# Kernel tuning notes

Measured on AMD Instinct MI355X. Metric: run time of the kernel, lower is better.

Reference implementation:

```python
import jax, jax.numpy as jnp
import numpy as np

N = 50000      # nodes
E = 800000     # edges
D_IN = 512
D_OUT = 512
EDGE_DIM = 3


def setup_inputs() -> dict:
    key = jax.random.key(0)
    k = jax.random.split(key, 6)
    x = jax.random.normal(k[0], (N, D_IN), dtype=jnp.float32)
    edge_index = jax.random.randint(k[1], (2, E), 0, N, dtype=jnp.int64)
    edge_attr = jax.random.normal(k[2], (E, EDGE_DIM), dtype=jnp.float32)
    # xavier-uniform-ish init for linear weights
    lim1 = (6.0 / (D_IN + D_OUT)) ** 0.5
    lin_w = jax.random.uniform(k[3], (D_OUT, D_IN), minval=-lim1, maxval=lim1, dtype=jnp.float32)
    lin_b = jnp.zeros((D_OUT,), dtype=jnp.float32)
    lim2 = (6.0 / (EDGE_DIM + 1)) ** 0.5
    conf_w = jax.random.uniform(k[4], (1, EDGE_DIM), minval=-lim2, maxval=lim2, dtype=jnp.float32)
    conf_b = jnp.zeros((1,), dtype=jnp.float32)
    return {"x": x, "edge_index": edge_index, "edge_attr": edge_attr,
            "lin_w": lin_w, "lin_b": lin_b, "conf_w": conf_w, "conf_b": conf_b}


def reference(x, edge_index, edge_attr, lin_w, lin_b, conf_w, conf_b):
    row, col = edge_index[0], edge_index[1]
    # edge confidence weight: sigmoid(conf_lin(edge_attr)) -> [E]
    edge_weight = jax.nn.sigmoid(edge_attr @ conf_w.T + conf_b)[:, 0]
    # degree of source nodes (count of row occurrences), inverse sqrt with inf/nan -> 0
    deg = jnp.zeros((x.shape[0],), dtype=x.dtype).at[row].add(1.0)
    deg_safe = jnp.where(deg > 0, deg, 1.0)
    deg_inv_sqrt = jnp.where(deg > 0, jax.lax.rsqrt(deg_safe), 0.0)
    norm = deg_inv_sqrt[row] * deg_inv_sqrt[col] * edge_weight  # [E]
    norm = jnp.where(jnp.isnan(norm), 0.0, norm)
    # gather-scale-scatter: out[col] += x[row] * norm
    out = jnp.zeros_like(x).at[col].add(x[row] * norm[:, None])
    return out @ lin_w.T + lin_b
```

## Files before the change

kernel.cpp:

```cpp
#include <hip/hip_runtime.h>

#define NDIM 512

typedef __bf16 bf16x8 __attribute__((ext_vector_type(8)));
typedef float  f32x4  __attribute__((ext_vector_type(4)));

__device__ inline ushort f2bf(float f) {
    uint b = __float_as_uint(f);
    return (ushort)((b + 0x7fffu + ((b >> 16) & 1u)) >> 16);
}
__device__ inline float bflo(uint u) { return __uint_as_float(u << 16); }
__device__ inline float bfhi(uint u) { return __uint_as_float(u & 0xffff0000u); }
__device__ inline uint packbf(float lo, float hi) {
    return ((uint)f2bf(hi) << 16) | (uint)f2bf(lo);
}

__device__ inline void gload16(const ushort* g, ushort* l) {
    __builtin_amdgcn_global_load_lds(
        (const __attribute__((address_space(1))) uint*)g,
        (__attribute__((address_space(3))) uint*)l, 16, 0, 0);
}

__global__ __launch_bounds__(256) void f2bf_kernel(const float* __restrict__ in,
                                                   ushort* __restrict__ out, int n4) {
    int i = blockIdx.x * 256 + threadIdx.x;
    if (i >= n4) return;
    float4 v = ((const float4*)in)[i];
    ushort4 o;
    o.x = f2bf(v.x); o.y = f2bf(v.y); o.z = f2bf(v.z); o.w = f2bf(v.w);
    ((ushort4*)out)[i] = o;
}

__global__ __launch_bounds__(256) void hist_kernel(const int* __restrict__ ei,
                                                   int* __restrict__ deg_row,
                                                   int* __restrict__ cnt_col, int E) {
    int e = blockIdx.x * 256 + threadIdx.x;
    if (e < E) {
        atomicAdd(&deg_row[ei[e]], 1);
        atomicAdd(&cnt_col[ei[E + e]], 1);
    }
}

__global__ __launch_bounds__(256) void rsqrt_kernel(const int* __restrict__ deg,
                                                    float* __restrict__ dis, int n) {
    int i = blockIdx.x * 256 + threadIdx.x;
    if (i < n) {
        int d = deg[i];
        dis[i] = (d > 0) ? rsqrtf((float)d) : 0.0f;
    }
}

__global__ __launch_bounds__(1024) void scan_kernel(const int* __restrict__ cnt,
                                                    int* __restrict__ base,
                                                    int* __restrict__ fc, int n) {
    __shared__ int wsum[16];
    __shared__ int carry_s;
    int tid = threadIdx.x;
    int lane = tid & 63, wid = tid >> 6;
    if (tid == 0) carry_s = 0;
    __syncthreads();
    for (int s = 0; s < n; s += 4096) {
        int i0 = s + tid * 4;
        int v0 = 0, v1 = 0, v2 = 0, v3 = 0;
        if (i0 + 3 < n) {
            int4 q = *(const int4*)(cnt + i0);
            v0 = q.x; v1 = q.y; v2 = q.z; v3 = q.w;
        } else if (i0 < n) {
            v0 = cnt[i0];
            if (i0 + 1 < n) v1 = cnt[i0 + 1];
            if (i0 + 2 < n) v2 = cnt[i0 + 2];
        }
        v0 = (v0 + 7) & ~7; v1 = (v1 + 7) & ~7;
        v2 = (v2 + 7) & ~7; v3 = (v3 + 7) & ~7;
        int tsum = v0 + v1 + v2 + v3;
        int incl = tsum;
#pragma unroll
        for (int off = 1; off < 64; off <<= 1) {
            int t = __shfl_up(incl, off, 64);
            if (lane >= off) incl += t;
        }
        if (lane == 63) wsum[wid] = incl;
        __syncthreads();
        int add = carry_s;
#pragma unroll
        for (int w = 0; w < 16; ++w) if (w < wid) add += wsum[w];
        int run = add + incl - tsum;
        if (i0 + 0 < n) { base[i0 + 0] = run; fc[i0 + 0] = run; } run += v0;
        if (i0 + 1 < n) { base[i0 + 1] = run; fc[i0 + 1] = run; } run += v1;
        if (i0 + 2 < n) { base[i0 + 2] = run; fc[i0 + 2] = run; } run += v2;
        if (i0 + 3 < n) { base[i0 + 3] = run; fc[i0 + 3] = run; }
        __syncthreads();
        if (tid == 1023) carry_s = add + incl;
        __syncthreads();
    }
    if (tid == 0) base[n] = carry_s;
}

__global__ __launch_bounds__(256) void fill_kernel(
        const int* __restrict__ ei, const float* __restrict__ ea,
        const float* __restrict__ dis,
        const float* __restrict__ conf_w, const float* __restrict__ conf_b,
        int* __restrict__ fill_cnt, int2* __restrict__ rn_sorted, int E) {
    int e = blockIdx.x * 256 + threadIdx.x;
    if (e >= E) return;
    int row = ei[e];
    int col = ei[E + e];
    float w = ea[(size_t)e*3+0]*conf_w[0] + ea[(size_t)e*3+1]*conf_w[1]
            + ea[(size_t)e*3+2]*conf_w[2] + conf_b[0];
    w = 1.0f / (1.0f + __expf(-w));
    float nm = dis[row] * dis[col] * w;
    int pos = atomicAdd(&fill_cnt[col], 1);
    rn_sorted[pos] = make_int2(row, __float_as_int(nm));
}

#define ACC8(u, nm)                                                     \
    a0 = fmaf(bflo((u).x), (nm), a0); a1 = fmaf(bfhi((u).x), (nm), a1); \
    a2 = fmaf(bflo((u).y), (nm), a2); a3 = fmaf(bfhi((u).y), (nm), a3); \
    a4 = fmaf(bflo((u).z), (nm), a4); a5 = fmaf(bfhi((u).z), (nm), a5); \
    a6 = fmaf(bflo((u).w), (nm), a6); a7 = fmaf(bfhi((u).w), (nm), a7);

__global__ __launch_bounds__(256) void agg_kernel(
        const ushort* __restrict__ xh, const int2* __restrict__ rn,
        const int* __restrict__ base, ushort* __restrict__ aggh, int N) {
    int wid  = threadIdx.x >> 6;
    int lane = threadIdx.x & 63;
    int node = blockIdx.x * 4 + wid;
    if (node >= N) return;
    int start = base[node], end = base[node + 1];
    const ushort* xc = xh + lane * 8;
    float a0 = 0.f, a1 = 0.f, a2 = 0.f, a3 = 0.f;
    float a4 = 0.f, a5 = 0.f, a6 = 0.f, a7 = 0.f;
    int p = start;
    if (p < end) {
        int2 e0 = rn[p+0], e1 = rn[p+1], e2 = rn[p+2], e3 = rn[p+3];
        int2 e4 = rn[p+4], e5 = rn[p+5], e6 = rn[p+6], e7 = rn[p+7];
        for (;;) {
            uint4 u0 = *(const uint4*)(xc + ((size_t)e0.x << 9));
            uint4 u1 = *(const uint4*)(xc + ((size_t)e1.x << 9));
            uint4 u2 = *(const uint4*)(xc + ((size_t)e2.x << 9));
            uint4 u3 = *(const uint4*)(xc + ((size_t)e3.x << 9));
            uint4 u4 = *(const uint4*)(xc + ((size_t)e4.x << 9));
            uint4 u5 = *(const uint4*)(xc + ((size_t)e5.x << 9));
            uint4 u6 = *(const uint4*)(xc + ((size_t)e6.x << 9));
            uint4 u7 = *(const uint4*)(xc + ((size_t)e7.x << 9));
            p += 8;
            int q = (p < end) ? p : start;
            int2 f0 = rn[q+0], f1 = rn[q+1], f2 = rn[q+2], f3 = rn[q+3];
            int2 f4 = rn[q+4], f5 = rn[q+5], f6 = rn[q+6], f7 = rn[q+7];
            float n0 = __int_as_float(e0.y), n1 = __int_as_float(e1.y);
            float n2 = __int_as_float(e2.y), n3 = __int_as_float(e3.y);
            float n4 = __int_as_float(e4.y), n5 = __int_as_float(e5.y);
            float n6 = __int_as_float(e6.y), n7 = __int_as_float(e7.y);
            ACC8(u0, n0); ACC8(u1, n1); ACC8(u2, n2); ACC8(u3, n3);
            ACC8(u4, n4); ACC8(u5, n5); ACC8(u6, n6); ACC8(u7, n7);
            if (p >= end) break;
            e0 = f0; e1 = f1; e2 = f2; e3 = f3;
            e4 = f4; e5 = f5; e6 = f6; e7 = f7;
        }
    }
    uint4 o;
    o.x = packbf(a0, a1);
    o.y = packbf(a2, a3);
    o.z = packbf(a4, a5);
    o.w = packbf(a6, a7);
    *(uint4*)(aggh + (size_t)node * NDIM + lane * 8) = o;
}

__global__ __launch_bounds__(256) void mfma_gemm(
        const ushort* __restrict__ A,
        const ushort* __restrict__ B,
        const float* __restrict__ bias,
        float* __restrict__ out, int M) {
    __shared__ ushort As[128 * 32];
    __shared__ ushort Bs[128 * 32];
    int Mb = (M + 127) >> 7;
    int lin = blockIdx.x;
    int full = (Mb >> 3) << 5;
    int mb, nb;
    if (lin < full) {
        mb = ((lin >> 5) << 3) + (lin & 7);
        nb = (lin >> 3) & 3;
    } else {
        int r = lin - full;
        int mrem = Mb & 7;
        mb = ((Mb >> 3) << 3) + (r % mrem);
        nb = r / mrem;
    }
    int m0 = mb << 7;
    int n0 = nb << 7;
    int tid  = threadIdx.x;
    int lane = tid & 63;
    int wave = tid >> 6;
    int wr = wave >> 1, wc = wave & 1;
    int quad = lane >> 4, l16 = lane & 15;
    int lrow = lane >> 2, lcol = (lane & 3) << 3;

    f32x4 acc[4][4] = {};

    for (int k0 = 0; k0 < NDIM; k0 += 32) {
#pragma unroll
        for (int i = 0; i < 2; ++i) {
            int ch = wave * 2 + i;
            int r  = ch * 16 + lrow;
            int gm = m0 + r; if (gm >= M) gm = M - 1;
            gload16(A + ((size_t)gm << 9) + k0 + lcol, &As[ch * 512]);
            gload16(B + ((size_t)(n0 + r) << 9) + k0 + lcol, &Bs[ch * 512]);
        }
        __syncthreads();
#pragma unroll
        for (int mt = 0; mt < 4; ++mt) {
            bf16x8 a = *(const bf16x8*)&As[(wr * 64 + mt * 16 + l16) * 32 + quad * 8];
#pragma unroll
            for (int nt = 0; nt < 4; ++nt) {
                bf16x8 b = *(const bf16x8*)&Bs[(wc * 64 + nt * 16 + l16) * 32 + quad * 8];
                acc[mt][nt] = __builtin_amdgcn_mfma_f32_16x16x32_bf16(a, b, acc[mt][nt], 0, 0, 0);
            }
        }
        __syncthreads();
    }
#pragma unroll
    for (int mt = 0; mt < 4; ++mt) {
#pragma unroll
        for (int nt = 0; nt < 4; ++nt) {
            int gn = n0 + wc * 64 + nt * 16 + l16;
            float bv = bias[gn];
#pragma unroll
            for (int r = 0; r < 4; ++r) {
                int gm = m0 + wr * 64 + mt * 16 + quad * 4 + r;
                if (gm < M) out[(size_t)gm * NDIM + gn] = acc[mt][nt][r] + bv;
            }
        }
    }
}

extern "C" void kernel_launch(void* const* d_in, const int* in_sizes, int n_in,
                              void* d_out, int out_size, void* d_ws, size_t ws_size,
                              hipStream_t stream) {
    const float* x      = (const float*)d_in[0];
    const int*   ei     = (const int*)  d_in[1];
    const float* ea     = (const float*)d_in[2];
    const float* lin_w  = (const float*)d_in[3];
    const float* lin_b  = (const float*)d_in[4];
    const float* conf_w = (const float*)d_in[5];
    const float* conf_b = (const float*)d_in[6];
    float* out = (float*)d_out;

    int N = in_sizes[0] / NDIM;
    int E = in_sizes[2] / 3;

    char* p = (char*)d_ws;
    auto alloc = [&](size_t bytes) {
        char* q = p;
        p += (bytes + 255) & ~(size_t)255;
        return q;
    };
    ushort* aggh       = (ushort*)alloc((size_t)N * NDIM * sizeof(ushort));
    ushort* wh         = (ushort*)alloc((size_t)NDIM * NDIM * sizeof(ushort));
    int*   deg_row     = (int*)  alloc((size_t)N * sizeof(int));
    int*   cnt_col     = (int*)  alloc((size_t)N * sizeof(int));
    int*   fill_cnt    = (int*)  alloc((size_t)N * sizeof(int));
    float* dis         = (float*)alloc((size_t)N * sizeof(float));
    int*   base        = (int*)  alloc((size_t)(N + 1) * sizeof(int));
    size_t rn_cap      = (size_t)E + 7 * (size_t)N + 8;
    int2*  rn_sorted   = (int2*) alloc(rn_cap * sizeof(int2));

    ushort* xh = (ushort*)d_out;

    size_t zero_bytes = (size_t)((char*)(rn_sorted + rn_cap) - (char*)deg_row);
    (void)hipMemsetAsync(deg_row, 0, zero_bytes, stream);

    int gE = (E + 255) / 256;
    int gN = (N + 255) / 256;
    int x4 = (N * NDIM) / 4, w4 = (NDIM * NDIM) / 4;
    f2bf_kernel  <<<(x4 + 255) / 256, 256, 0, stream>>>(x, xh, x4);
    f2bf_kernel  <<<(w4 + 255) / 256, 256, 0, stream>>>(lin_w, wh, w4);
    hist_kernel  <<<gE, 256, 0, stream>>>(ei, deg_row, cnt_col, E);
    rsqrt_kernel <<<gN, 256, 0, stream>>>(deg_row, dis, N);
    scan_kernel  <<<1, 1024, 0, stream>>>(cnt_col, base, fill_cnt, N);
    fill_kernel  <<<gE, 256, 0, stream>>>(ei, ea, dis, conf_w, conf_b,
                                          fill_cnt, rn_sorted, E);
    agg_kernel   <<<(N + 3) / 4, 256, 0, stream>>>(xh, rn_sorted, base, aggh, N);
    int Mb = (N + 127) >> 7;
    mfma_gemm    <<<Mb * 4, 256, 0, stream>>>(aggh, wh, lin_b, out, N);
}
```

Before: 504.9 us.

## Fuse prep kernels, inline rsqrt into fill, stage gathers via LDS async loads

Merges the two bf16 conversions and the degree histogram into one launch, and computes the inverse-sqrt degrees inside the fill kernel so the separate rsqrt pass and its buffer go away. The aggregation kernel now reads edge entries as int4 pairs and gathers neighbor rows with global_load_lds into a per-wave LDS staging buffer before accumulating. This cuts launch count and is meant to improve memory-level parallelism in the gather. The cost is 32KB of LDS per block, which may lower occupancy. The LDS reads also rely on implicit wave-local ordering, with no explicit wait or barrier visible.

```diff
diff --git a/kernel.cpp b/kernel.cpp
--- a/kernel.cpp
+++ b/kernel.cpp
@@ -21,32 +21,35 @@
         (__attribute__((address_space(3))) uint*)l, 16, 0, 0);
 }
 
-__global__ __launch_bounds__(256) void f2bf_kernel(const float* __restrict__ in,
-                                                   ushort* __restrict__ out, int n4) {
-    int i = blockIdx.x * 256 + threadIdx.x;
-    if (i >= n4) return;
-    float4 v = ((const float4*)in)[i];
-    ushort4 o;
-    o.x = f2bf(v.x); o.y = f2bf(v.y); o.z = f2bf(v.z); o.w = f2bf(v.w);
-    ((ushort4*)out)[i] = o;
-}
-
-__global__ __launch_bounds__(256) void hist_kernel(const int* __restrict__ ei,
-                                                   int* __restrict__ deg_row,
-                                                   int* __restrict__ cnt_col, int E) {
-    int e = blockIdx.x * 256 + threadIdx.x;
-    if (e < E) {
-        atomicAdd(&deg_row[ei[e]], 1);
-        atomicAdd(&cnt_col[ei[E + e]], 1);
-    }
-}
-
-__global__ __launch_bounds__(256) void rsqrt_kernel(const int* __restrict__ deg,
-                                                    float* __restrict__ dis, int n) {
-    int i = blockIdx.x * 256 + threadIdx.x;
-    if (i < n) {
-        int d = deg[i];
-        dis[i] = (d > 0) ? rsqrtf((float)d) : 0.0f;
+__global__ __launch_bounds__(256) void prep_kernel(
+        const float* __restrict__ x,  ushort* __restrict__ xh,
+        const float* __restrict__ w,  ushort* __restrict__ wh,
+        const int* __restrict__ ei, int* __restrict__ deg_row,
+        int* __restrict__ cnt_col,
+        int nx4, int nw4, int E, int gX, int gW) {
+    int b = blockIdx.x;
+    if (b < gX) {
+        int i = b * 256 + threadIdx.x;
+        if (i < nx4) {
+            float4 v = ((const float4*)x)[i];
+            ushort4 o;
+            o.x = f2bf(v.x); o.y = f2bf(v.y); o.z = f2bf(v.z); o.w = f2bf(v.w);
+            ((ushort4*)xh)[i] = o;
+        }
+    } else if (b < gX + gW) {
+        int i = (b - gX) * 256 + threadIdx.x;
+        if (i < nw4) {
+            float4 v = ((const float4*)w)[i];
+            ushort4 o;
+            o.x = f2bf(v.x); o.y = f2bf(v.y); o.z = f2bf(v.z); o.w = f2bf(v.w);
+            ((ushort4*)wh)[i] = o;
+        }
+    } else {
+        int e = (b - gX - gW) * 256 + threadIdx.x;
+        if (e < E) {
+            atomicAdd(&deg_row[ei[e]], 1);
+            atomicAdd(&cnt_col[ei[E + e]], 1);
+        }
     }
 }
 
@@ -98,7 +101,7 @@
 
 __global__ __launch_bounds__(256) void fill_kernel(
         const int* __restrict__ ei, const float* __restrict__ ea,
-        const float* __restrict__ dis,
+        const int* __restrict__ deg,
         const float* __restrict__ conf_w, const float* __restrict__ conf_b,
         int* __restrict__ fill_cnt, int2* __restrict__ rn_sorted, int E) {
     int e = blockIdx.x * 256 + threadIdx.x;
@@ -108,7 +111,10 @@
     float w = ea[(size_t)e*3+0]*conf_w[0] + ea[(size_t)e*3+1]*conf_w[1]
             + ea[(size_t)e*3+2]*conf_w[2] + conf_b[0];
     w = 1.0f / (1.0f + __expf(-w));
-    float nm = dis[row] * dis[col] * w;
+    int dr = deg[row], dc = deg[col];
+    float ir = (dr > 0) ? rsqrtf((float)dr) : 0.0f;
+    float ic = (dc > 0) ? rsqrtf((float)dc) : 0.0f;
+    float nm = ir * ic * w;
     int pos = atomicAdd(&fill_cnt[col], 1);
     rn_sorted[pos] = make_int2(row, __float_as_int(nm));
 }
@@ -122,40 +128,52 @@
 __global__ __launch_bounds__(256) void agg_kernel(
         const ushort* __restrict__ xh, const int2* __restrict__ rn,
         const int* __restrict__ base, ushort* __restrict__ aggh, int N) {
+    __shared__ ushort stage[4 * 8 * 512];
     int wid  = threadIdx.x >> 6;
     int lane = threadIdx.x & 63;
     int node = blockIdx.x * 4 + wid;
     if (node >= N) return;
     int start = base[node], end = base[node + 1];
-    const ushort* xc = xh + lane * 8;
+    ushort* buf = stage + wid * (8 * 512);
+    const size_t loff = (size_t)lane * 8;
     float a0 = 0.f, a1 = 0.f, a2 = 0.f, a3 = 0.f;
     float a4 = 0.f, a5 = 0.f, a6 = 0.f, a7 = 0.f;
     int p = start;
     if (p < end) {
-        int2 e0 = rn[p+0], e1 = rn[p+1], e2 = rn[p+2], e3 = rn[p+3];
-        int2 e4 = rn[p+4], e5 = rn[p+5], e6 = rn[p+6], e7 = rn[p+7];
+        int4 q0 = *(const int4*)(rn + p + 0);
+        int4 q1 = *(const int4*)(rn + p + 2);
+        int4 q2 = *(const int4*)(rn + p + 4);
+        int4 q3 = *(const int4*)(rn + p + 6);
         for (;;) {
-            uint4 u0 = *(const uint4*)(xc + ((size_t)e0.x << 9));
-            uint4 u1 = *(const uint4*)(xc + ((size_t)e1.x << 9));
-            uint4 u2 = *(const uint4*)(xc + ((size_t)e2.x << 9));
-            uint4 u3 = *(const uint4*)(xc + ((size_t)e3.x << 9));
-            uint4 u4 = *(const uint4*)(xc + ((size_t)e4.x << 9));
-            uint4 u5 = *(const uint4*)(xc + ((size_t)e5.x << 9));
-            uint4 u6 = *(const uint4*)(xc + ((size_t)e6.x << 9));
-            uint4 u7 = *(const uint4*)(xc + ((size_t)e7.x << 9));
+            gload16(xh + ((size_t)(uint)q0.x << 9) + loff, buf + 0 * 512);
+            gload16(xh + ((size_t)(uint)q0.z << 9) + loff, buf + 1 * 512);
+            gload16(xh + ((size_t)(uint)q1.x << 9) + loff, buf + 2 * 512);
+            gload16(xh + ((size_t)(uint)q1.z << 9) + loff, buf + 3 * 512);
+            gload16(xh + ((size_t)(uint)q2.x << 9) + loff, buf + 4 * 512);
+            gload16(xh + ((size_t)(uint)q2.z << 9) + loff, buf + 5 * 512);
+            gload16(xh + ((size_t)(uint)q3.x << 9) + loff, buf + 6 * 512);
+            gload16(xh + ((size_t)(uint)q3.z << 9) + loff, buf + 7 * 512);
+            float n0 = __int_as_float(q0.y), n1 = __int_as_float(q0.w);
+            float n2 = __int_as_float(q1.y), n3 = __int_as_float(q1.w);
+            float n4 = __int_as_float(q2.y), n5 = __int_as_float(q2.w);
+            float n6 = __int_as_float(q3.y), n7 = __int_as_float(q3.w);
             p += 8;
-            int q = (p < end) ? p : start;
-            int2 f0 = rn[q+0], f1 = rn[q+1], f2 = rn[q+2], f3 = rn[q+3];
-            int2 f4 = rn[q+4], f5 = rn[q+5], f6 = rn[q+6], f7 = rn[q+7];
-            float n0 = __int_as_float(e0.y), n1 = __int_as_float(e1.y);
-            float n2 = __int_as_float(e2.y), n3 = __int_as_float(e3.y);
-            float n4 = __int_as_float(e4.y), n5 = __int_as_float(e5.y);
-            float n6 = __int_as_float(e6.y), n7 = __int_as_float(e7.y);
-            ACC8(u0, n0); ACC8(u1, n1); ACC8(u2, n2); ACC8(u3, n3);
-            ACC8(u4, n4); ACC8(u5, n5); ACC8(u6, n6); ACC8(u7, n7);
-            if (p >= end) break;
-            e0 = f0; e1 = f1; e2 = f2; e3 = f3;
-            e4 = f4; e5 = f5; e6 = f6; e7 = f7;
+            bool more = p < end;
+            int q = more ? p : start;
+            q0 = *(const int4*)(rn + q + 0);
+            q1 = *(const int4*)(rn + q + 2);
+            q2 = *(const int4*)(rn + q + 4);
+            q3 = *(const int4*)(rn + q + 6);
+            uint4 u;
+            u = *(const uint4*)(buf + 0 * 512 + loff); ACC8(u, n0);
+            u = *(const uint4*)(buf + 1 * 512 + loff); ACC8(u, n1);
+            u = *(const uint4*)(buf + 2 * 512 + loff); ACC8(u, n2);
+            u = *(const uint4*)(buf + 3 * 512 + loff); ACC8(u, n3);
+            u = *(const uint4*)(buf + 4 * 512 + loff); ACC8(u, n4);
+            u = *(const uint4*)(buf + 5 * 512 + loff); ACC8(u, n5);
+            u = *(const uint4*)(buf + 6 * 512 + loff); ACC8(u, n6);
+            u = *(const uint4*)(buf + 7 * 512 + loff); ACC8(u, n7);
+            if (!more) break;
         }
     }
     uint4 o;
@@ -163,7 +181,7 @@
     o.y = packbf(a2, a3);
     o.z = packbf(a4, a5);
     o.w = packbf(a6, a7);
-    *(uint4*)(aggh + (size_t)node * NDIM + lane * 8) = o;
+    *(uint4*)(aggh + (size_t)node * NDIM + loff) = o;
 }
 
 __global__ __launch_bounds__(256) void mfma_gemm(
@@ -259,7 +277,6 @@
     int*   deg_row     = (int*)  alloc((size_t)N * sizeof(int));
     int*   cnt_col     = (int*)  alloc((size_t)N * sizeof(int));
     int*   fill_cnt    = (int*)  alloc((size_t)N * sizeof(int));
-    float* dis         = (float*)alloc((size_t)N * sizeof(float));
     int*   base        = (int*)  alloc((size_t)(N + 1) * sizeof(int));
     size_t rn_cap      = (size_t)E + 7 * (size_t)N + 8;
     int2*  rn_sorted   = (int2*) alloc(rn_cap * sizeof(int2));
@@ -270,14 +287,12 @@
     (void)hipMemsetAsync(deg_row, 0, zero_bytes, stream);
 
     int gE = (E + 255) / 256;
-    int gN = (N + 255) / 256;
     int x4 = (N * NDIM) / 4, w4 = (NDIM * NDIM) / 4;
-    f2bf_kernel  <<<(x4 + 255) / 256, 256, 0, stream>>>(x, xh, x4);
-    f2bf_kernel  <<<(w4 + 255) / 256, 256, 0, stream>>>(lin_w, wh, w4);
-    hist_kernel  <<<gE, 256, 0, stream>>>(ei, deg_row, cnt_col, E);
-    rsqrt_kernel <<<gN, 256, 0, stream>>>(deg_row, dis, N);
+    int gX = (x4 + 255) / 256, gW = (w4 + 255) / 256;
+    prep_kernel  <<<gX + gW + gE, 256, 0, stream>>>(x, xh, lin_w, wh, ei,
+                                                    deg_row, cnt_col, x4, w4, E, gX, gW);
     scan_kernel  <<<1, 1024, 0, stream>>>(cnt_col, base, fill_cnt, N);
-    fill_kernel  <<<gE, 256, 0, stream>>>(ei, ea, dis, conf_w, conf_b,
+    fill_kernel  <<<gE, 256, 0, stream>>>(ei, ea, deg_row, conf_w, conf_b,
                                           fill_cnt, rn_sorted, E);
     agg_kernel   <<<(N + 3) / 4, 256, 0, stream>>>(xh, rn_sorted, base, aggh, N);
     int Mb = (N + 127) >> 7;
```

Measured after the change: 495.9 us. No clear change (-1.8%).
